# Kernel optimization log

Hardware: AMD Instinct MI355X
Metric: run time of the kernel (lower is better)

## Reference

```python
import jax, jax.numpy as jnp
import numpy as np

N_NODES = 50000
N_EDGES = 800000
D_IN, D_HID, D_OUT, D_EDGE = 128, 256, 128, 16


def setup_inputs() -> dict:
    key = jax.random.key(0)
    ks = jax.random.split(key, 6)
    nh = jax.random.normal(ks[0], (N_NODES, D_IN), dtype=jnp.float32)
    eh = jax.random.normal(ks[1], (N_EDGES, D_EDGE), dtype=jnp.float32)
    edge_index = jax.random.randint(ks[2], (2, N_EDGES), 0, N_NODES, dtype=jnp.int32)
    # MLP params (build_layer: Linear(d_in,d_hid) -> relu -> Linear(d_hid,d_out)), scaled init
    W1 = jax.random.normal(ks[3], (D_IN, D_HID), dtype=jnp.float32) / np.sqrt(D_IN)
    b1 = jnp.zeros((D_HID,), dtype=jnp.float32)
    W2 = jax.random.normal(ks[4], (D_HID, D_OUT), dtype=jnp.float32) / np.sqrt(D_HID)
    b2 = jnp.zeros((D_OUT,), dtype=jnp.float32)
    return {"nh": nh, "eh": eh, "edge_index": edge_index,
            "W1": W1, "b1": b1, "W2": W2, "b2": b2}


def reference(nh, eh, edge_index, W1, b1, W2, b2):
    n_nodes = nh.shape[0]
    # nf_lin: 2-layer MLP with relu
    n_h = jax.nn.relu(nh @ W1 + b1) @ W2 + b2          # [N, d]
    src, dst = edge_index[0], edge_index[1]
    src_nh = n_h[src]                                   # [E, d] gather
    dst_nh = n_h[dst]                                   # [E, d] gather
    attn = jnp.sum(src_nh * dst_nh, axis=-1)            # [E] per-edge score
    # segment softmax over edges grouped by destination node
    seg_max = jax.ops.segment_max(attn, dst, num_segments=n_nodes)  # [N]
    e = jnp.exp(attn - seg_max[dst])                    # [E] stable exp
    denom = jax.ops.segment_sum(e, dst, num_segments=n_nodes)       # [N]
    attn = e / denom[dst]                               # [E]
    # weighted scatter-add aggregation
    nz = jax.ops.segment_sum(attn[:, None] * src_nh, dst, num_segments=n_nodes)  # [N, d]
    return (n_h + nz, eh)
```

## Files before the change

### kernel.cpp

```cpp
#include <hip/hip_runtime.h>
#include <math.h>


#define D_IN   128
#define D_HID  256
#define D_OUT  128

typedef short bf16x8 __attribute__((ext_vector_type(8)));
typedef float f32x4  __attribute__((ext_vector_type(4)));

__device__ __forceinline__ short f2bf(float f)
{
    unsigned int u = __float_as_uint(f);
    unsigned int r = (u + 0x7fffu + ((u >> 16) & 1u)) >> 16;
    return (short)r;
}
__device__ __forceinline__ float bf2f(short h)
{
    return __uint_as_float(((unsigned int)(unsigned short)h) << 16);
}

__device__ __forceinline__ void pack_body(const float* __restrict__ W,
                                          short* __restrict__ Bh,
                                          short* __restrict__ Bl,
                                          int K, int N, int u)
{
    const int T = K >> 5;
    const int l = u & 63;
    const int t = (u >> 6) % T;
    const int c = u / (64 * T);
    const int lr = l & 15, kb = l >> 4;
    bf16x8 vh, vl;
#pragma unroll
    for (int j = 0; j < 8; ++j) {
        int k   = t * 32 + kb * 8 + j;
        int col = c * 16 + lr;
        float x = W[(size_t)k * N + col];
        short hi = f2bf(x);
        vh[j] = hi;
        vl[j] = f2bf(x - bf2f(hi));
    }
    *(bf16x8*)(Bh + (size_t)u * 8) = vh;
    *(bf16x8*)(Bl + (size_t)u * 8) = vl;
}

__global__ __launch_bounds__(256)
void prep(const float* __restrict__ A, short* __restrict__ Ah,
          short* __restrict__ Al, long valid, long total8, int nAB,
          const float* __restrict__ W1, short* __restrict__ B1h,
          short* __restrict__ B1l,
          const float* __restrict__ W2, short* __restrict__ B2h,
          short* __restrict__ B2l)
{
    int b = blockIdx.x;
    const int tid = threadIdx.x;
    if (b < nAB) {
        long t = (long)b * 256 + tid;
        if (t < total8) {
            long base = t * 8;
            bf16x8 vh, vl;
            if (base < valid) {
                float4 f0 = *(const float4*)(A + base);
                float4 f1 = *(const float4*)(A + base + 4);
                float fv[8] = {f0.x, f0.y, f0.z, f0.w, f1.x, f1.y, f1.z, f1.w};
#pragma unroll
                for (int j = 0; j < 8; ++j) {
                    short hi = f2bf(fv[j]);
                    vh[j] = hi;
                    vl[j] = f2bf(fv[j] - bf2f(hi));
                }
            } else {
                vh = (bf16x8)0; vl = (bf16x8)0;
            }
            *(bf16x8*)(Ah + base) = vh;
            *(bf16x8*)(Al + base) = vl;
        }
        return;
    }
    b -= nAB;
    if (b < 16) pack_body(W1, B1h, B1l, D_IN, D_HID, b * 256 + tid);
    else        pack_body(W2, B2h, B2l, D_HID, D_OUT, (b - 16) * 256 + tid);
}

__global__ __launch_bounds__(256)
void hist_pos(const int* __restrict__ dst, unsigned int* __restrict__ count,
              unsigned int* __restrict__ pos, int E)
{
    int e = blockIdx.x * blockDim.x + threadIdx.x;
    if (e < E) pos[e] = atomicAdd(count + dst[e], 1u);
}

#define H2_STRIDE 264

__global__ __launch_bounds__(256)
void mlp_fused(const short* __restrict__ Ah, const short* __restrict__ Al,
               const short* __restrict__ B1h, const short* __restrict__ B1l,
               const float* __restrict__ b1,
               const short* __restrict__ B2h, const short* __restrict__ B2l,
               const float* __restrict__ b2,
               float* __restrict__ out, short* __restrict__ nhb, int Nvalid)
{
    __shared__ __attribute__((aligned(16))) short H[64 * H2_STRIDE];

    const int w  = threadIdx.x >> 6;
    const int l  = threadIdx.x & 63;
    const int lr = l & 15, kb = l >> 4;
    const size_t row0 = (size_t)blockIdx.x * 64;

    f32x4 acc1[4][4] = {};
#pragma unroll
    for (int t = 0; t < 4; ++t) {
        bf16x8 ah[4], al[4], bh[4], bl[4];
#pragma unroll
        for (int m = 0; m < 4; ++m) {
            size_t aoff = (row0 + m * 16 + lr) * D_IN + t * 32 + kb * 8;
            ah[m] = *(const bf16x8*)(Ah + aoff);
            al[m] = *(const bf16x8*)(Al + aoff);
        }
#pragma unroll
        for (int n = 0; n < 4; ++n) {
            int c = w * 4 + n;
            size_t boff = (size_t)((c * 4 + t) * 64 + l) * 8;
            bh[n] = *(const bf16x8*)(B1h + boff);
            bl[n] = *(const bf16x8*)(B1l + boff);
        }
#pragma unroll
        for (int m = 0; m < 4; ++m)
#pragma unroll
            for (int n = 0; n < 4; ++n) {
                acc1[m][n] = __builtin_amdgcn_mfma_f32_16x16x32_bf16(ah[m], bh[n], acc1[m][n], 0, 0, 0);
                acc1[m][n] = __builtin_amdgcn_mfma_f32_16x16x32_bf16(al[m], bh[n], acc1[m][n], 0, 0, 0);
                acc1[m][n] = __builtin_amdgcn_mfma_f32_16x16x32_bf16(ah[m], bl[n], acc1[m][n], 0, 0, 0);
            }
    }

#pragma unroll
    for (int n = 0; n < 4; ++n) {
        int col = w * 64 + n * 16 + lr;
        float bb = b1[col];
#pragma unroll
        for (int m = 0; m < 4; ++m)
#pragma unroll
            for (int i = 0; i < 4; ++i) {
                int lrow = m * 16 + kb * 4 + i;
                float v = fmaxf(acc1[m][n][i] + bb, 0.f);
                H[lrow * H2_STRIDE + col] = f2bf(v);
            }
    }
    __syncthreads();

    f32x4 acc2[4][2] = {};
#pragma unroll
    for (int t2 = 0; t2 < 8; ++t2) {
        bf16x8 a[4], bh[2], bl[2];
#pragma unroll
        for (int m = 0; m < 4; ++m)
            a[m] = *(const bf16x8*)&H[(m * 16 + lr) * H2_STRIDE + t2 * 32 + kb * 8];
#pragma unroll
        for (int n = 0; n < 2; ++n) {
            int c = w * 2 + n;
            size_t boff = (size_t)((c * 8 + t2) * 64 + l) * 8;
            bh[n] = *(const bf16x8*)(B2h + boff);
            bl[n] = *(const bf16x8*)(B2l + boff);
        }
#pragma unroll
        for (int m = 0; m < 4; ++m)
#pragma unroll
            for (int n = 0; n < 2; ++n) {
                acc2[m][n] = __builtin_amdgcn_mfma_f32_16x16x32_bf16(a[m], bh[n], acc2[m][n], 0, 0, 0);
                acc2[m][n] = __builtin_amdgcn_mfma_f32_16x16x32_bf16(a[m], bl[n], acc2[m][n], 0, 0, 0);
            }
    }

#pragma unroll
    for (int n = 0; n < 2; ++n) {
        int col = w * 32 + n * 16 + lr;
        float bb = b2[col];
#pragma unroll
        for (int m = 0; m < 4; ++m)
#pragma unroll
            for (int i = 0; i < 4; ++i) {
                size_t row = row0 + m * 16 + kb * 4 + i;
                float v = acc2[m][n][i] + bb;
                nhb[row * D_OUT + col] = f2bf(v);
                if ((int)row < Nvalid) out[row * D_OUT + col] = v;
            }
    }
}

__global__ __launch_bounds__(256)
void chunk_sums(const unsigned int* __restrict__ count,
                unsigned int* __restrict__ bsum, int n)
{
    __shared__ unsigned int lds[256];
    const int t = threadIdx.x;
    const int i = blockIdx.x * 256 + t;
    lds[t] = (i < n) ? count[i] : 0u;
    __syncthreads();
#pragma unroll
    for (int d = 128; d > 0; d >>= 1) {
        if (t < d) lds[t] += lds[t + d];
        __syncthreads();
    }
    if (t == 0) bsum[blockIdx.x] = lds[0];
}

__global__ __launch_bounds__(256)
void scan_sums(const unsigned int* __restrict__ bsum,
               unsigned int* __restrict__ boff, int nb)
{
    __shared__ unsigned int lds[256];
    const int t = threadIdx.x;
    unsigned int v = (t < nb) ? bsum[t] : 0u;
    lds[t] = v;
    __syncthreads();
#pragma unroll
    for (int d = 1; d < 256; d <<= 1) {
        unsigned int x = lds[t];
        unsigned int add = (t >= d) ? lds[t - d] : 0u;
        __syncthreads();
        lds[t] = x + add;
        __syncthreads();
    }
    if (t < nb) boff[t] = lds[t] - v;
}

__global__ __launch_bounds__(256)
void write_off(const unsigned int* __restrict__ count,
               const unsigned int* __restrict__ boff,
               unsigned int* __restrict__ off, int n)
{
    __shared__ unsigned int lds[256];
    const int t = threadIdx.x;
    const int i = blockIdx.x * 256 + t;
    unsigned int v = (i < n) ? count[i] : 0u;
    lds[t] = v;
    __syncthreads();
#pragma unroll
    for (int d = 1; d < 256; d <<= 1) {
        unsigned int x = lds[t];
        unsigned int add = (t >= d) ? lds[t - d] : 0u;
        __syncthreads();
        lds[t] = x + add;
        __syncthreads();
    }
    unsigned int incl = lds[t];
    unsigned int base = boff[blockIdx.x];
    if (i < n)  off[i] = base + incl - v;
    if (i == n - 1) off[n] = base + incl;
}

__global__ __launch_bounds__(256)
void fill_srcs(const int* __restrict__ src, const int* __restrict__ dst,
               const unsigned int* __restrict__ off,
               const unsigned int* __restrict__ pos,
               int* __restrict__ srcs, int E)
{
    int e = blockIdx.x * blockDim.x + threadIdx.x;
    if (e >= E) return;
    srcs[off[dst[e]] + pos[e]] = src[e];
}

#define NEG_HUGE -3.0e38f

__global__ __launch_bounds__(256)
void agg_copy(const short* __restrict__ nhb,
              const unsigned int* __restrict__ off,
              const int* __restrict__ srcs,
              float* __restrict__ out, int N,
              const float4* __restrict__ ehin, float4* __restrict__ ehout,
              int n4, int copyB)
{
    if ((int)blockIdx.x < copyB) {
        for (int i = blockIdx.x * 256 + threadIdx.x; i < n4; i += copyB * 256)
            ehout[i] = ehin[i];
        return;
    }
    int wid  = (((int)blockIdx.x - copyB) * 256 + (int)threadIdx.x) >> 6;
    int lane = threadIdx.x & 63;
    if (wid >= N) return;
    const int g = lane >> 4;
    const int j = lane & 15;

    const float* sp = out + (size_t)wid * D_OUT + j * 8;
    const float4 sa = *(const float4*)sp;
    const float4 sb = *(const float4*)(sp + 4);

    const unsigned int beg = off[wid];
    const unsigned int end = off[wid + 1];

    float m = NEG_HUGE, den = 0.f;
    float c0 = 0.f, c1 = 0.f, c2 = 0.f, c3 = 0.f;
    float c4 = 0.f, c5 = 0.f, c6 = 0.f, c7 = 0.f;

    for (unsigned int base = beg; base < end; base += 8) {
        unsigned int idx0 = base + g * 2;
        unsigned int idx1 = idx0 + 1;
        bool v0 = idx0 < end, v1 = idx1 < end;
        int s0 = v0 ? srcs[idx0] : 0;
        int s1 = v1 ? srcs[idx1] : 0;
        uint4 A0 = *(const uint4*)(nhb + (size_t)s0 * D_OUT + j * 8);
        uint4 A1 = *(const uint4*)(nhb + (size_t)s1 * D_OUT + j * 8);

        float a00 = __uint_as_float(A0.x << 16), a01 = __uint_as_float(A0.x & 0xffff0000u);
        float a02 = __uint_as_float(A0.y << 16), a03 = __uint_as_float(A0.y & 0xffff0000u);
        float a04 = __uint_as_float(A0.z << 16), a05 = __uint_as_float(A0.z & 0xffff0000u);
        float a06 = __uint_as_float(A0.w << 16), a07 = __uint_as_float(A0.w & 0xffff0000u);
        float a10 = __uint_as_float(A1.x << 16), a11 = __uint_as_float(A1.x & 0xffff0000u);
        float a12 = __uint_as_float(A1.y << 16), a13 = __uint_as_float(A1.y & 0xffff0000u);
        float a14 = __uint_as_float(A1.z << 16), a15 = __uint_as_float(A1.z & 0xffff0000u);
        float a16 = __uint_as_float(A1.w << 16), a17 = __uint_as_float(A1.w & 0xffff0000u);

        float p0 = a00 * sa.x + a01 * sa.y + a02 * sa.z + a03 * sa.w
                 + a04 * sb.x + a05 * sb.y + a06 * sb.z + a07 * sb.w;
        float p1 = a10 * sa.x + a11 * sa.y + a12 * sa.z + a13 * sa.w
                 + a14 * sb.x + a15 * sb.y + a16 * sb.z + a17 * sb.w;
        p0 += __shfl_xor(p0, 1);  p1 += __shfl_xor(p1, 1);
        p0 += __shfl_xor(p0, 2);  p1 += __shfl_xor(p1, 2);
        p0 += __shfl_xor(p0, 4);  p1 += __shfl_xor(p1, 4);
        p0 += __shfl_xor(p0, 8);  p1 += __shfl_xor(p1, 8);

        float p0v = v0 ? p0 : NEG_HUGE;
        float p1v = v1 ? p1 : NEG_HUGE;
        float mnew = fmaxf(m, fmaxf(p0v, p1v));
        float scale = __expf(m - mnew);
        float w0 = v0 ? __expf(p0 - mnew) : 0.f;
        float w1 = v1 ? __expf(p1 - mnew) : 0.f;
        den = fmaf(den, scale, w0 + w1);
        c0 = fmaf(c0, scale, fmaf(w0, a00, w1 * a10));
        c1 = fmaf(c1, scale, fmaf(w0, a01, w1 * a11));
        c2 = fmaf(c2, scale, fmaf(w0, a02, w1 * a12));
        c3 = fmaf(c3, scale, fmaf(w0, a03, w1 * a13));
        c4 = fmaf(c4, scale, fmaf(w0, a04, w1 * a14));
        c5 = fmaf(c5, scale, fmaf(w0, a05, w1 * a15));
        c6 = fmaf(c6, scale, fmaf(w0, a06, w1 * a16));
        c7 = fmaf(c7, scale, fmaf(w0, a07, w1 * a17));
        m = mnew;
    }

#pragma unroll
    for (int o = 16; o < 64; o <<= 1) {
        float m2 = __shfl_xor(m, o);
        float d2 = __shfl_xor(den, o);
        float b0 = __shfl_xor(c0, o), b1 = __shfl_xor(c1, o);
        float b2v = __shfl_xor(c2, o), b3 = __shfl_xor(c3, o);
        float b4 = __shfl_xor(c4, o), b5 = __shfl_xor(c5, o);
        float b6 = __shfl_xor(c6, o), b7 = __shfl_xor(c7, o);
        float mn = fmaxf(m, m2);
        float s1 = __expf(m - mn);
        float s2 = __expf(m2 - mn);
        den = den * s1 + d2 * s2;
        c0 = c0 * s1 + b0 * s2;  c1 = c1 * s1 + b1 * s2;
        c2 = c2 * s1 + b2v * s2; c3 = c3 * s1 + b3 * s2;
        c4 = c4 * s1 + b4 * s2;  c5 = c5 * s1 + b5 * s2;
        c6 = c6 * s1 + b6 * s2;  c7 = c7 * s1 + b7 * s2;
        m = mn;
    }

    float inv = (den > 0.f) ? 1.f / den : 0.f;
    if (g == 0) {
        float4 o0, o1;
        o0.x = sa.x + c0 * inv; o0.y = sa.y + c1 * inv;
        o0.z = sa.z + c2 * inv; o0.w = sa.w + c3 * inv;
        o1.x = sb.x + c4 * inv; o1.y = sb.y + c5 * inv;
        o1.z = sb.z + c6 * inv; o1.w = sb.w + c7 * inv;
        float* op = out + (size_t)wid * D_OUT + j * 8;
        *(float4*)op = o0;
        *(float4*)(op + 4) = o1;
    }
}

extern "C" void kernel_launch(void* const* d_in, const int* in_sizes, int n_in,
                              void* d_out, int out_size, void* d_ws, size_t ws_size,
                              hipStream_t stream)
{
    const float* nh  = (const float*)d_in[0];
    const float* eh  = (const float*)d_in[1];
    const int*   ei  = (const int*)d_in[2];
    const float* W1  = (const float*)d_in[3];
    const float* b1  = (const float*)d_in[4];
    const float* W2  = (const float*)d_in[5];
    const float* b2  = (const float*)d_in[6];

    const int N  = in_sizes[0] / D_IN;
    const int E  = in_sizes[2] / 2;
    const int EH = in_sizes[1];
    const int Mp = (N + 63) & ~63;
    const int NB = (N + 255) / 256;

    const int* src = ei;
    const int* dst = ei + E;

    float* out_nh = (float*)d_out;
    float* out_eh = (float*)d_out + (size_t)N * D_OUT;

    char* ws = (char*)d_ws;
    size_t o = 0;
    short* Ahp = (short*)(ws + o); o += (size_t)Mp * D_IN * 2;
    short* Alp = (short*)(ws + o); o += (size_t)Mp * D_IN * 2;
    short* nhb = (short*)(ws + o); o += (size_t)Mp * D_OUT * 2;
    short* B1h = (short*)(ws + o); o += (size_t)D_IN  * D_HID * 2;
    short* B1l = (short*)(ws + o); o += (size_t)D_IN  * D_HID * 2;
    short* B2h = (short*)(ws + o); o += (size_t)D_HID * D_OUT * 2;
    short* B2l = (short*)(ws + o); o += (size_t)D_HID * D_OUT * 2;
    int*          srcs  = (int*)(ws + o);          o += (size_t)E * 4;
    unsigned int* pos   = (unsigned int*)(ws + o); o += (size_t)E * 4;
    unsigned int* count = (unsigned int*)(ws + o); o += (size_t)N * 4;
    unsigned int* off   = (unsigned int*)(ws + o); o += (size_t)(N + 1) * 4;
    unsigned int* bsum  = (unsigned int*)(ws + o); o += (size_t)NB * 4;
    unsigned int* boff  = (unsigned int*)(ws + o); o += (size_t)NB * 4;

    hipMemsetAsync(count, 0, (size_t)N * 4, stream);
    {
        long total8 = (long)Mp * D_IN / 8;
        int  nAB    = (int)((total8 + 255) / 256);
        prep<<<nAB + 32, 256, 0, stream>>>(
            nh, Ahp, Alp, (long)N * D_IN, total8, nAB,
            W1, B1h, B1l, W2, B2h, B2l);
    }

    hist_pos<<<(E + 255) / 256, 256, 0, stream>>>(dst, count, pos, E);
    chunk_sums<<<NB, 256, 0, stream>>>(count, bsum, N);
    scan_sums<<<1, 256, 0, stream>>>(bsum, boff, NB);
    write_off<<<NB, 256, 0, stream>>>(count, boff, off, N);
    fill_srcs<<<(E + 255) / 256, 256, 0, stream>>>(src, dst, off, pos, srcs, E);

    mlp_fused<<<Mp / 64, 256, 0, stream>>>(Ahp, Alp, B1h, B1l, b1,
                                           B2h, B2l, b2, out_nh, nhb, N);

    {
        int copyB = 512;
        int aggB  = (N + 3) / 4;
        agg_copy<<<copyB + aggB, 256, 0, stream>>>(
            nhb, off, srcs, out_nh, N,
            (const float4*)eh, (float4*)out_eh, EH / 4, copyB);
    }
}
```

Baseline: 160.8 us.

## Fold count memset into prep, merge scan kernels, use 8 waves in MLP

The separate memset of the per-node count array moves into extra blocks of the prep kernel. The three-kernel prefix scan becomes a single scan_all kernel in which each block recomputes its base by summing all preceding counts. The fused MLP kernel now runs 512 threads as a 2x4 grid of waves, so each wave handles half the rows. The goal is fewer launches and more waves per MLP tile, but the scan's prefix recompute is quadratic in block count, so later blocks read up to the whole count array.

```diff
diff --git a/kernel.cpp b/kernel.cpp
--- a/kernel.cpp
+++ b/kernel.cpp
@@ -50,7 +50,8 @@
           const float* __restrict__ W1, short* __restrict__ B1h,
           short* __restrict__ B1l,
           const float* __restrict__ W2, short* __restrict__ B2h,
-          short* __restrict__ B2l)
+          short* __restrict__ B2l,
+          unsigned int* __restrict__ count, int N)
 {
     int b = blockIdx.x;
     const int tid = threadIdx.x;
@@ -78,8 +79,14 @@
         return;
     }
     b -= nAB;
-    if (b < 16) pack_body(W1, B1h, B1l, D_IN, D_HID, b * 256 + tid);
-    else        pack_body(W2, B2h, B2l, D_HID, D_OUT, (b - 16) * 256 + tid);
+    if (b < 32) {
+        if (b < 16) pack_body(W1, B1h, B1l, D_IN, D_HID, b * 256 + tid);
+        else        pack_body(W2, B2h, B2l, D_HID, D_OUT, (b - 16) * 256 + tid);
+        return;
+    }
+    b -= 32;
+    int i = b * 256 + tid;
+    if (i < N) count[i] = 0u;
 }
 
 __global__ __launch_bounds__(256)
@@ -90,9 +97,57 @@
     if (e < E) pos[e] = atomicAdd(count + dst[e], 1u);
 }
 
+__global__ __launch_bounds__(256)
+void scan_all(const unsigned int* __restrict__ count,
+              unsigned int* __restrict__ off, int n)
+{
+    __shared__ unsigned int lds[256];
+    const int t = threadIdx.x;
+    const int b = blockIdx.x;
+
+    unsigned int s = 0;
+    for (int i = t; i < b * 256; i += 256) s += count[i];
+    lds[t] = s;
+    __syncthreads();
+#pragma unroll
+    for (int d = 128; d > 0; d >>= 1) {
+        if (t < d) lds[t] += lds[t + d];
+        __syncthreads();
+    }
+    unsigned int base = lds[0];
+    __syncthreads();
+
+    int i = b * 256 + t;
+    unsigned int v = (i < n) ? count[i] : 0u;
+    lds[t] = v;
+    __syncthreads();
+#pragma unroll
+    for (int d = 1; d < 256; d <<= 1) {
+        unsigned int x = lds[t];
+        unsigned int add = (t >= d) ? lds[t - d] : 0u;
+        __syncthreads();
+        lds[t] = x + add;
+        __syncthreads();
+    }
+    unsigned int incl = lds[t];
+    if (i < n)      off[i] = base + incl - v;
+    if (i == n - 1) off[n] = base + incl;
+}
+
+__global__ __launch_bounds__(256)
+void fill_srcs(const int* __restrict__ src, const int* __restrict__ dst,
+               const unsigned int* __restrict__ off,
+               const unsigned int* __restrict__ pos,
+               int* __restrict__ srcs, int E)
+{
+    int e = blockIdx.x * blockDim.x + threadIdx.x;
+    if (e >= E) return;
+    srcs[off[dst[e]] + pos[e]] = src[e];
+}
+
 #define H2_STRIDE 264
 
-__global__ __launch_bounds__(256)
+__global__ __launch_bounds__(512)
 void mlp_fused(const short* __restrict__ Ah, const short* __restrict__ Al,
                const short* __restrict__ B1h, const short* __restrict__ B1l,
                const float* __restrict__ b1,
@@ -105,27 +160,29 @@
     const int w  = threadIdx.x >> 6;
     const int l  = threadIdx.x & 63;
     const int lr = l & 15, kb = l >> 4;
+    const int wr = w >> 2;
+    const int wc = w & 3;
     const size_t row0 = (size_t)blockIdx.x * 64;
 
-    f32x4 acc1[4][4] = {};
+    f32x4 acc1[2][4] = {};
 #pragma unroll
     for (int t = 0; t < 4; ++t) {
-        bf16x8 ah[4], al[4], bh[4], bl[4];
-#pragma unroll
-        for (int m = 0; m < 4; ++m) {
-            size_t aoff = (row0 + m * 16 + lr) * D_IN + t * 32 + kb * 8;
+        bf16x8 ah[2], al[2], bh[4], bl[4];
+#pragma unroll
+        for (int m = 0; m < 2; ++m) {
+            size_t aoff = (row0 + wr * 32 + m * 16 + lr) * D_IN + t * 32 + kb * 8;
             ah[m] = *(const bf16x8*)(Ah + aoff);
             al[m] = *(const bf16x8*)(Al + aoff);
         }
 #pragma unroll
         for (int n = 0; n < 4; ++n) {
-            int c = w * 4 + n;
+            int c = wc * 4 + n;
             size_t boff = (size_t)((c * 4 + t) * 64 + l) * 8;
             bh[n] = *(const bf16x8*)(B1h + boff);
             bl[n] = *(const bf16x8*)(B1l + boff);
         }
 #pragma unroll
-        for (int m = 0; m < 4; ++m)
+        for (int m = 0; m < 2; ++m)
 #pragma unroll
             for (int n = 0; n < 4; ++n) {
                 acc1[m][n] = __builtin_amdgcn_mfma_f32_16x16x32_bf16(ah[m], bh[n], acc1[m][n], 0, 0, 0);
@@ -136,35 +193,35 @@
 
 #pragma unroll
     for (int n = 0; n < 4; ++n) {
-        int col = w * 64 + n * 16 + lr;
+        int col = wc * 64 + n * 16 + lr;
         float bb = b1[col];
 #pragma unroll
-        for (int m = 0; m < 4; ++m)
+        for (int m = 0; m < 2; ++m)
 #pragma unroll
             for (int i = 0; i < 4; ++i) {
-                int lrow = m * 16 + kb * 4 + i;
+                int lrow = wr * 32 + m * 16 + kb * 4 + i;
                 float v = fmaxf(acc1[m][n][i] + bb, 0.f);
                 H[lrow * H2_STRIDE + col] = f2bf(v);
             }
     }
     __syncthreads();
 
-    f32x4 acc2[4][2] = {};
+    f32x4 acc2[2][2] = {};
 #pragma unroll
     for (int t2 = 0; t2 < 8; ++t2) {
-        bf16x8 a[4], bh[2], bl[2];
-#pragma unroll
-        for (int m = 0; m < 4; ++m)
-            a[m] = *(const bf16x8*)&H[(m * 16 + lr) * H2_STRIDE + t2 * 32 + kb * 8];
+        bf16x8 a[2], bh[2], bl[2];
+#pragma unroll
+        for (int m = 0; m < 2; ++m)
+            a[m] = *(const bf16x8*)&H[(wr * 32 + m * 16 + lr) * H2_STRIDE + t2 * 32 + kb * 8];
 #pragma unroll
         for (int n = 0; n < 2; ++n) {
-            int c = w * 2 + n;
+            int c = wc * 2 + n;
             size_t boff = (size_t)((c * 8 + t2) * 64 + l) * 8;
             bh[n] = *(const bf16x8*)(B2h + boff);
             bl[n] = *(const bf16x8*)(B2l + boff);
         }
 #pragma unroll
-        for (int m = 0; m < 4; ++m)
+        for (int m = 0; m < 2; ++m)
 #pragma unroll
             for (int n = 0; n < 2; ++n) {
                 acc2[m][n] = __builtin_amdgcn_mfma_f32_16x16x32_bf16(a[m], bh[n], acc2[m][n], 0, 0, 0);
@@ -174,91 +231,18 @@
 
 #pragma unroll
     for (int n = 0; n < 2; ++n) {
-        int col = w * 32 + n * 16 + lr;
+        int col = wc * 32 + n * 16 + lr;
         float bb = b2[col];
 #pragma unroll
-        for (int m = 0; m < 4; ++m)
+        for (int m = 0; m < 2; ++m)
 #pragma unroll
             for (int i = 0; i < 4; ++i) {
-                size_t row = row0 + m * 16 + kb * 4 + i;
+                size_t row = row0 + wr * 32 + m * 16 + kb * 4 + i;
                 float v = acc2[m][n][i] + bb;
                 nhb[row * D_OUT + col] = f2bf(v);
                 if ((int)row < Nvalid) out[row * D_OUT + col] = v;
             }
     }
-}
-
-__global__ __launch_bounds__(256)
-void chunk_sums(const unsigned int* __restrict__ count,
-                unsigned int* __restrict__ bsum, int n)
-{
-    __shared__ unsigned int lds[256];
-    const int t = threadIdx.x;
-    const int i = blockIdx.x * 256 + t;
-    lds[t] = (i < n) ? count[i] : 0u;
-    __syncthreads();
-#pragma unroll
-    for (int d = 128; d > 0; d >>= 1) {
-        if (t < d) lds[t] += lds[t + d];
-        __syncthreads();
-    }
-    if (t == 0) bsum[blockIdx.x] = lds[0];
-}
-
-__global__ __launch_bounds__(256)
-void scan_sums(const unsigned int* __restrict__ bsum,
-               unsigned int* __restrict__ boff, int nb)
-{
-    __shared__ unsigned int lds[256];
-    const int t = threadIdx.x;
-    unsigned int v = (t < nb) ? bsum[t] : 0u;
-    lds[t] = v;
-    __syncthreads();
-#pragma unroll
-    for (int d = 1; d < 256; d <<= 1) {
-        unsigned int x = lds[t];
-        unsigned int add = (t >= d) ? lds[t - d] : 0u;
-        __syncthreads();
-        lds[t] = x + add;
-        __syncthreads();
-    }
-    if (t < nb) boff[t] = lds[t] - v;
-}
-
-__global__ __launch_bounds__(256)
-void write_off(const unsigned int* __restrict__ count,
-               const unsigned int* __restrict__ boff,
-               unsigned int* __restrict__ off, int n)
-{
-    __shared__ unsigned int lds[256];
-    const int t = threadIdx.x;
-    const int i = blockIdx.x * 256 + t;
-    unsigned int v = (i < n) ? count[i] : 0u;
-    lds[t] = v;
-    __syncthreads();
-#pragma unroll
-    for (int d = 1; d < 256; d <<= 1) {
-        unsigned int x = lds[t];
-        unsigned int add = (t >= d) ? lds[t - d] : 0u;
-        __syncthreads();
-        lds[t] = x + add;
-        __syncthreads();
-    }
-    unsigned int incl = lds[t];
-    unsigned int base = boff[blockIdx.x];
-    if (i < n)  off[i] = base + incl - v;
-    if (i == n - 1) off[n] = base + incl;
-}
-
-__global__ __launch_bounds__(256)
-void fill_srcs(const int* __restrict__ src, const int* __restrict__ dst,
-               const unsigned int* __restrict__ off,
-               const unsigned int* __restrict__ pos,
-               int* __restrict__ srcs, int E)
-{
-    int e = blockIdx.x * blockDim.x + threadIdx.x;
-    if (e >= E) return;
-    srcs[off[dst[e]] + pos[e]] = src[e];
 }
 
 #define NEG_HUGE -3.0e38f
@@ -407,25 +391,20 @@
     unsigned int* pos   = (unsigned int*)(ws + o); o += (size_t)E * 4;
     unsigned int* count = (unsigned int*)(ws + o); o += (size_t)N * 4;
     unsigned int* off   = (unsigned int*)(ws + o); o += (size_t)(N + 1) * 4;
-    unsigned int* bsum  = (unsigned int*)(ws + o); o += (size_t)NB * 4;
-    unsigned int* boff  = (unsigned int*)(ws + o); o += (size_t)NB * 4;
-
-    hipMemsetAsync(count, 0, (size_t)N * 4, stream);
+
     {
         long total8 = (long)Mp * D_IN / 8;
         int  nAB    = (int)((total8 + 255) / 256);
-        prep<<<nAB + 32, 256, 0, stream>>>(
+        prep<<<nAB + 32 + NB, 256, 0, stream>>>(
             nh, Ahp, Alp, (long)N * D_IN, total8, nAB,
-            W1, B1h, B1l, W2, B2h, B2l);
+            W1, B1h, B1l, W2, B2h, B2l, count, N);
     }
 
     hist_pos<<<(E + 255) / 256, 256, 0, stream>>>(dst, count, pos, E);
-    chunk_sums<<<NB, 256, 0, stream>>>(count, bsum, N);
-    scan_sums<<<1, 256, 0, stream>>>(bsum, boff, NB);
-    write_off<<<NB, 256, 0, stream>>>(count, boff, off, N);
+    scan_all<<<NB, 256, 0, stream>>>(count, off, N);
     fill_srcs<<<(E + 255) / 256, 256, 0, stream>>>(src, dst, off, pos, srcs, E);
 
-    mlp_fused<<<Mp / 64, 256, 0, stream>>>(Ahp, Alp, B1h, B1l, b1,
+    mlp_fused<<<Mp / 64, 512, 0, stream>>>(Ahp, Alp, B1h, B1l, b1,
                                            B2h, B2l, b2, out_nh, nhb, N);
 
     {
```

Result: slower. 178.6 us (+11.1%).
